# Kernel tuning notes

Measured on AMD Instinct MI355X. Metric: run time of the kernel, lower is better.

Reference implementation:

```python
import jax, jax.numpy as jnp
import numpy as np

KERNEL = 4
STRIDE = 2
PADDING = 1


def setup_inputs() -> dict:
    key = jax.random.key(0)
    k1, k2, k3 = jax.random.split(key, 3)
    x = jax.random.normal(k1, (256, 128, 128), dtype=jnp.float32)
    W = jax.random.normal(k2, (128, 256, KERNEL, KERNEL), dtype=jnp.float32) * 0.02
    b = jax.random.normal(k3, (128,), dtype=jnp.float32) * 0.02
    return {"x": x, "W": W, "b": b}


def reference(x, W, b):
    # Original: zero-insert x with stride 2 (at[:, ::2].set), pad by
    # (kernel - padding - 1) on each spatial side, then dense stride-1 conv.
    # lhs_dilation=STRIDE performs the identical zero-insertion (size 2H-1)
    # without materializing the sparse intermediate; padding matches jnp.pad.
    pad = KERNEL - PADDING - 1  # = 2
    out = jax.lax.conv_general_dilated(
        x[None],  # (1, C_in, H, W)
        W,        # (C_out, C_in, k, k), cross-correlation as in equinox Conv2d
        window_strides=(1, 1),
        padding=((pad, pad), (pad, pad)),
        lhs_dilation=(STRIDE, STRIDE),
        dimension_numbers=("NCHW", "OIHW", "NCHW"),
    )[0]
    return out + b[:, None, None]
```

## Files before the change

### kernel.cpp

```cpp
#include <hip/hip_runtime.h>


typedef __attribute__((ext_vector_type(8))) short bf16x8;
typedef __attribute__((ext_vector_type(16))) float f32x16;

#define CI 256
#define CO 128
#define HW 128
#define YO_TILE 4
#define XO_TILE 16
#define CELLS_R 6
#define CELLS_C 18
#define NCELLS (CELLS_R * CELLS_C)
#define LDS_BYTES (NCELLS * 512)

static __device__ __forceinline__ unsigned short f2bf(float f) {
  union { float f; unsigned u; } v; v.f = f;
  return (unsigned short)((v.u + 0x7FFFu + ((v.u >> 16) & 1u)) >> 16);
}

__global__ void transpose_x_kernel(const float* __restrict__ x,
                                   unsigned short* __restrict__ xbT) {
  __shared__ float tile[32][33];
  const int hw0 = blockIdx.x * 32;
  const int ci0 = blockIdx.y * 32;
  const int tx = threadIdx.x;
  const int ty = threadIdx.y;
#pragma unroll
  for (int i = 0; i < 4; ++i) {
    const int ci = ci0 + ty + i * 8;
    tile[ty + i * 8][tx] = x[ci * (HW * HW) + hw0 + tx];
  }
  __syncthreads();
#pragma unroll
  for (int i = 0; i < 4; ++i) {
    const int hw = hw0 + ty + i * 8;
    xbT[hw * CI + ci0 + tx] = f2bf(tile[tx][ty + i * 8]);
  }
}

__global__ void reorg_w_kernel(const float* __restrict__ W,
                               unsigned short* __restrict__ Wb) {
  const int tid = blockIdx.x * 256 + threadIdx.x;
  const int ci_lo = tid & 15;
  const int o     = (tid >> 4) & 127;
  const int cbG   = (tid >> 11) & 15;
  const int tap   = (tid >> 15) & 15;
  const int ci = cbG * 16 + ci_lo;
  Wb[tid] = f2bf(W[(o * CI + ci) * 16 + tap]);
}

__global__ __launch_bounds__(512, 2) void tconv_mfma_kernel(
    const unsigned short* __restrict__ xbT,
    const unsigned short* __restrict__ Wb,
    const float* __restrict__ bias,
    float* __restrict__ out) {
  __shared__ __align__(16) unsigned char LDS[LDS_BYTES];
  const int tid = threadIdx.x;
  const int X0 = blockIdx.x * XO_TILE;
  const int Y0 = blockIdx.y * YO_TILE;

  for (int e = tid; e < NCELLS * 32; e += 512) {
    const int s = e & 31;
    const int cell = e >> 5;
    const int c = cell % CELLS_C;
    const int r = cell / CELLS_C;
    const int gr = Y0 - 1 + r;
    const int gc = X0 - 1 + c;
    uint4 val = make_uint4(0u, 0u, 0u, 0u);
    if (gr >= 0 && gr < HW && gc >= 0 && gc < HW)
      val = *(const uint4*)(xbT + ((gr * HW + gc) * CI + s * 8));
    *(uint4*)(LDS + cell * 512 + ((s ^ c) * 16)) = val;
  }
  __syncthreads();

  const int lane = tid & 63;
  const int wave = tid >> 6;
  const int cls = wave & 3;
  const int ry = cls >> 1, rx = cls & 1;
  const int kh2 = wave >> 2;
  const int l31 = lane & 31;
  const int lhi = lane >> 5;
  const int nrow = l31 >> 4;
  const int ncol = l31 & 15;

  f32x16 acc[4][2];
#pragma unroll
  for (int mt = 0; mt < 4; ++mt)
#pragma unroll
    for (int nt = 0; nt < 2; ++nt)
#pragma unroll
      for (int t = 0; t < 16; ++t) acc[mt][nt][t] = 0.0f;

#pragma unroll
  for (int a = 0; a < 2; ++a) {
#pragma unroll
    for (int b = 0; b < 2; ++b) {
      const int tap = (2 * a + ry) * 4 + (2 * b + rx);
      const int c_l = ncol + rx + b;
      const int r_base = nrow + ry + a;
      const unsigned short* wtap = Wb + tap * 16 * 2048;
#pragma unroll
      for (int cb = 0; cb < 8; ++cb) {
        const int cbG = kh2 * 8 + cb;
        const int s_idx = cbG * 2 + lhi;
        bf16x8 bfrag[2];
#pragma unroll
        for (int nt = 0; nt < 2; ++nt) {
          const int cell = (r_base + 2 * nt) * CELLS_C + c_l;
          bfrag[nt] = *(const bf16x8*)(LDS + cell * 512 + ((s_idx ^ c_l) * 16));
        }
        const unsigned short* wk = wtap + cbG * 2048 + l31 * 16 + lhi * 8;
#pragma unroll
        for (int mt = 0; mt < 4; ++mt) {
          const bf16x8 afrag = *(const bf16x8*)(wk + mt * 512);
#pragma unroll
          for (int nt = 0; nt < 2; ++nt)
            acc[mt][nt] = __builtin_amdgcn_mfma_f32_32x32x16_bf16(
                afrag, bfrag[nt], acc[mt][nt], 0, 0, 0);
        }
      }
    }
  }

  __syncthreads();
  float* red = (float*)LDS;
#pragma unroll
  for (int round = 0; round < 4; ++round) {
    const int nt = round >> 1;
    const int oh = round & 1;
    if (kh2 == 1) {
#pragma unroll
      for (int m2 = 0; m2 < 2; ++m2) {
        const f32x16 v = acc[oh * 2 + m2][nt];
#pragma unroll
        for (int t = 0; t < 16; ++t) {
          const int o_l = m2 * 32 + (t & 3) + 4 * lhi + 8 * (t >> 2);
          red[(cls * 64 + o_l) * 32 + l31] = v[t];
        }
      }
    }
    __syncthreads();
    if (kh2 == 0) {
#pragma unroll
      for (int m2 = 0; m2 < 2; ++m2) {
        const f32x16 v = acc[oh * 2 + m2][nt];
#pragma unroll
        for (int t = 0; t < 16; ++t) {
          const int rowD = (t & 3) + 4 * lhi + 8 * (t >> 2);
          const int o_l = m2 * 32 + rowD;
          const int o = oh * 64 + o_l;
          const float sum = v[t] + red[(cls * 64 + o_l) * 32 + l31] + bias[o];
          const int yo = Y0 + nt * 2 + nrow;
          const int xo = X0 + ncol;
          const int y = 2 * yo + ry;
          const int xg = 2 * xo + rx;
          out[((size_t)o << 16) + (y << 8) + xg] = sum;
        }
      }
    }
    __syncthreads();
  }
}

extern "C" void kernel_launch(void* const* d_in, const int* in_sizes, int n_in,
                              void* d_out, int out_size, void* d_ws, size_t ws_size,
                              hipStream_t stream) {
  const float* x = (const float*)d_in[0];
  const float* W = (const float*)d_in[1];
  const float* b = (const float*)d_in[2];
  float* out = (float*)d_out;

  unsigned short* xbT = (unsigned short*)d_ws;
  unsigned short* Wb = xbT + (size_t)CI * HW * HW;

  transpose_x_kernel<<<dim3((HW * HW) / 32, CI / 32), dim3(32, 8), 0, stream>>>(x, xbT);
  reorg_w_kernel<<<dim3((16 * 16 * CO * 16) / 256), dim3(256), 0, stream>>>(W, Wb);
  tconv_mfma_kernel<<<dim3(HW / XO_TILE, HW / YO_TILE), dim3(512), 0, stream>>>(xbT, Wb, b, out);
}
```

Measured before the change: 105.4 us.

## Split MFMA work by output-channel and row halves, drop K-split reduction

The main conv kernel now uses 1024 threads per block. Waves split the output channels and the output rows instead of splitting the input-channel reduction, so the LDS cross-wave reduction and its barriers go away and each wave writes its results directly. The transpose and weight-reorg prep kernels are also vectorized with float4 loads and 16-byte stores. In exchange, each wave now re-reads weight fragments from global memory for the full K dimension, and the per-wave accumulator footprint changes, which affects register pressure and occupancy.

```diff
diff --git a/kernel.cpp b/kernel.cpp
--- a/kernel.cpp
+++ b/kernel.cpp
@@ -19,38 +19,50 @@
   return (unsigned short)((v.u + 0x7FFFu + ((v.u >> 16) & 1u)) >> 16);
 }
 
-__global__ void transpose_x_kernel(const float* __restrict__ x,
-                                   unsigned short* __restrict__ xbT) {
-  __shared__ float tile[32][33];
-  const int hw0 = blockIdx.x * 32;
-  const int ci0 = blockIdx.y * 32;
-  const int tx = threadIdx.x;
-  const int ty = threadIdx.y;
+__global__ __launch_bounds__(256) void transpose_x_kernel(const float* __restrict__ x,
+                                                          unsigned short* __restrict__ xbT) {
+  __shared__ unsigned short tileT[64][68];
+  const int hw0 = blockIdx.x * 64;
+  const int ci0 = blockIdx.y * 64;
+  const int tid = threadIdx.x;
 #pragma unroll
-  for (int i = 0; i < 4; ++i) {
-    const int ci = ci0 + ty + i * 8;
-    tile[ty + i * 8][tx] = x[ci * (HW * HW) + hw0 + tx];
+  for (int it = 0; it < 4; ++it) {
+    const int p = it * 256 + tid;
+    const int ci_r = p >> 4;
+    const int c4 = p & 15;
+    const float4 v = *(const float4*)(x + (size_t)(ci0 + ci_r) * (HW * HW) + hw0 + c4 * 4);
+    tileT[c4 * 4 + 0][ci_r] = f2bf(v.x);
+    tileT[c4 * 4 + 1][ci_r] = f2bf(v.y);
+    tileT[c4 * 4 + 2][ci_r] = f2bf(v.z);
+    tileT[c4 * 4 + 3][ci_r] = f2bf(v.w);
   }
   __syncthreads();
 #pragma unroll
-  for (int i = 0; i < 4; ++i) {
-    const int hw = hw0 + ty + i * 8;
-    xbT[hw * CI + ci0 + tx] = f2bf(tile[tx][ty + i * 8]);
+  for (int it = 0; it < 2; ++it) {
+    const int p = it * 256 + tid;
+    const int cg = p & 7;
+    const int hw = p >> 3;
+    const bf16x8 v = *(const bf16x8*)&tileT[hw][cg * 8];
+    *(bf16x8*)(xbT + (size_t)(hw0 + hw) * CI + ci0 + cg * 8) = v;
   }
 }
 
-__global__ void reorg_w_kernel(const float* __restrict__ W,
-                               unsigned short* __restrict__ Wb) {
+__global__ __launch_bounds__(256) void reorg_w_kernel(const float* __restrict__ W,
+                                                      unsigned short* __restrict__ Wb) {
   const int tid = blockIdx.x * 256 + threadIdx.x;
-  const int ci_lo = tid & 15;
-  const int o     = (tid >> 4) & 127;
-  const int cbG   = (tid >> 11) & 15;
-  const int tap   = (tid >> 15) & 15;
-  const int ci = cbG * 16 + ci_lo;
-  Wb[tid] = f2bf(W[(o * CI + ci) * 16 + tap]);
+  const int f = tid * 4;
+  const int tap0 = f & 15;
+  const int ci = (f >> 4) & 255;
+  const int o = f >> 12;
+  const float4 v = *(const float4*)(W + f);
+  const int base = ((ci >> 4) * CO + o) * 16 + (ci & 15);
+  Wb[(tap0 + 0) * 32768 + base] = f2bf(v.x);
+  Wb[(tap0 + 1) * 32768 + base] = f2bf(v.y);
+  Wb[(tap0 + 2) * 32768 + base] = f2bf(v.z);
+  Wb[(tap0 + 3) * 32768 + base] = f2bf(v.w);
 }
 
-__global__ __launch_bounds__(512, 2) void tconv_mfma_kernel(
+__global__ __launch_bounds__(1024, 4) void tconv_mfma_kernel(
     const unsigned short* __restrict__ xbT,
     const unsigned short* __restrict__ Wb,
     const float* __restrict__ bias,
@@ -60,7 +72,7 @@
   const int X0 = blockIdx.x * XO_TILE;
   const int Y0 = blockIdx.y * YO_TILE;
 
-  for (int e = tid; e < NCELLS * 32; e += 512) {
+  for (int e = tid; e < NCELLS * 32; e += 1024) {
     const int s = e & 31;
     const int cell = e >> 5;
     const int c = cell % CELLS_C;
@@ -78,19 +90,18 @@
   const int wave = tid >> 6;
   const int cls = wave & 3;
   const int ry = cls >> 1, rx = cls & 1;
-  const int kh2 = wave >> 2;
+  const int mh = (wave >> 2) & 1;
+  const int sph = wave >> 3;
   const int l31 = lane & 31;
   const int lhi = lane >> 5;
   const int nrow = l31 >> 4;
   const int ncol = l31 & 15;
 
-  f32x16 acc[4][2];
+  f32x16 acc[2];
 #pragma unroll
-  for (int mt = 0; mt < 4; ++mt)
+  for (int mt = 0; mt < 2; ++mt)
 #pragma unroll
-    for (int nt = 0; nt < 2; ++nt)
-#pragma unroll
-      for (int t = 0; t < 16; ++t) acc[mt][nt][t] = 0.0f;
+    for (int t = 0; t < 16; ++t) acc[mt][t] = 0.0f;
 
 #pragma unroll
   for (int a = 0; a < 2; ++a) {
@@ -98,69 +109,34 @@
     for (int b = 0; b < 2; ++b) {
       const int tap = (2 * a + ry) * 4 + (2 * b + rx);
       const int c_l = ncol + rx + b;
-      const int r_base = nrow + ry + a;
-      const unsigned short* wtap = Wb + tap * 16 * 2048;
+      const int r_base = sph * 2 + nrow + ry + a;
+      const int cellbase = (r_base * CELLS_C + c_l) * 512;
+      const unsigned short* wt = Wb + tap * 32768 + (mh * 64 + l31) * 16 + lhi * 8;
 #pragma unroll
-      for (int cb = 0; cb < 8; ++cb) {
-        const int cbG = kh2 * 8 + cb;
-        const int s_idx = cbG * 2 + lhi;
-        bf16x8 bfrag[2];
+      for (int cb = 0; cb < 16; ++cb) {
+        const int s_idx = cb * 2 + lhi;
+        const bf16x8 bfrag = *(const bf16x8*)(LDS + cellbase + ((s_idx ^ c_l) * 16));
+        const unsigned short* wk = wt + cb * 2048;
 #pragma unroll
-        for (int nt = 0; nt < 2; ++nt) {
-          const int cell = (r_base + 2 * nt) * CELLS_C + c_l;
-          bfrag[nt] = *(const bf16x8*)(LDS + cell * 512 + ((s_idx ^ c_l) * 16));
-        }
-        const unsigned short* wk = wtap + cbG * 2048 + l31 * 16 + lhi * 8;
-#pragma unroll
-        for (int mt = 0; mt < 4; ++mt) {
-          const bf16x8 afrag = *(const bf16x8*)(wk + mt * 512);
-#pragma unroll
-          for (int nt = 0; nt < 2; ++nt)
-            acc[mt][nt] = __builtin_amdgcn_mfma_f32_32x32x16_bf16(
-                afrag, bfrag[nt], acc[mt][nt], 0, 0, 0);
-        }
+        for (int mt = 0; mt < 2; ++mt)
+          acc[mt] = __builtin_amdgcn_mfma_f32_32x32x16_bf16(
+              *(const bf16x8*)(wk + mt * 512), bfrag, acc[mt], 0, 0, 0);
       }
     }
   }
 
-  __syncthreads();
-  float* red = (float*)LDS;
+  const int yo = Y0 + sph * 2 + nrow;
+  const int xo = X0 + ncol;
+  const int y = 2 * yo + ry;
+  const int xg = 2 * xo + rx;
 #pragma unroll
-  for (int round = 0; round < 4; ++round) {
-    const int nt = round >> 1;
-    const int oh = round & 1;
-    if (kh2 == 1) {
+  for (int mt = 0; mt < 2; ++mt)
 #pragma unroll
-      for (int m2 = 0; m2 < 2; ++m2) {
-        const f32x16 v = acc[oh * 2 + m2][nt];
-#pragma unroll
-        for (int t = 0; t < 16; ++t) {
-          const int o_l = m2 * 32 + (t & 3) + 4 * lhi + 8 * (t >> 2);
-          red[(cls * 64 + o_l) * 32 + l31] = v[t];
-        }
-      }
+    for (int t = 0; t < 16; ++t) {
+      const int rowD = (t & 3) + 4 * lhi + 8 * (t >> 2);
+      const int o = mh * 64 + mt * 32 + rowD;
+      out[((size_t)o << 16) + (y << 8) + xg] = acc[mt][t] + bias[o];
     }
-    __syncthreads();
-    if (kh2 == 0) {
-#pragma unroll
-      for (int m2 = 0; m2 < 2; ++m2) {
-        const f32x16 v = acc[oh * 2 + m2][nt];
-#pragma unroll
-        for (int t = 0; t < 16; ++t) {
-          const int rowD = (t & 3) + 4 * lhi + 8 * (t >> 2);
-          const int o_l = m2 * 32 + rowD;
-          const int o = oh * 64 + o_l;
-          const float sum = v[t] + red[(cls * 64 + o_l) * 32 + l31] + bias[o];
-          const int yo = Y0 + nt * 2 + nrow;
-          const int xo = X0 + ncol;
-          const int y = 2 * yo + ry;
-          const int xg = 2 * xo + rx;
-          out[((size_t)o << 16) + (y << 8) + xg] = sum;
-        }
-      }
-    }
-    __syncthreads();
-  }
 }
 
 extern "C" void kernel_launch(void* const* d_in, const int* in_sizes, int n_in,
@@ -174,7 +150,7 @@
   unsigned short* xbT = (unsigned short*)d_ws;
   unsigned short* Wb = xbT + (size_t)CI * HW * HW;
 
-  transpose_x_kernel<<<dim3((HW * HW) / 32, CI / 32), dim3(32, 8), 0, stream>>>(x, xbT);
-  reorg_w_kernel<<<dim3((16 * 16 * CO * 16) / 256), dim3(256), 0, stream>>>(W, Wb);
-  tconv_mfma_kernel<<<dim3(HW / XO_TILE, HW / YO_TILE), dim3(512), 0, stream>>>(xbT, Wb, b, out);
+  transpose_x_kernel<<<dim3((HW * HW) / 64, CI / 64), dim3(256), 0, stream>>>(x, xbT);
+  reorg_w_kernel<<<dim3(512), dim3(256), 0, stream>>>(W, Wb);
+  tconv_mfma_kernel<<<dim3(HW / XO_TILE, HW / YO_TILE), dim3(1024), 0, stream>>>(xbT, Wb, b, out);
 }
```

After: 108.2 us. 2.7% more time.
